# Performance work log

Measured on AMD Instinct MI355X. Metric: run time of the kernel, lower is better.

The kernel has to match this reference:

```python
import jax, jax.numpy as jnp
import numpy as np
from jax import lax

B, N, C, H = 32, 1025, 512, 8
HD = C // H            # head dim = 64
HS = WS = 32           # feature map size, N = 1 + HS*WS
SCALE = HD ** -0.5
SPLITS = (128, 192, 192)  # window {3:2,5:3,7:3} * head_dim


def setup_inputs() -> dict:
    key = jax.random.key(0)
    ks = jax.random.split(key, 11)
    return {
        "x": jax.random.normal(ks[0], (B, N, C), jnp.float32),
        "Wqkv": jax.random.normal(ks[1], (C, 3 * C), jnp.float32) * 0.02,
        "bqkv": jnp.zeros((3 * C,), jnp.float32),
        "Wproj": jax.random.normal(ks[2], (C, C), jnp.float32) * 0.02,
        "bproj": jnp.zeros((C,), jnp.float32),
        "ck3": jax.random.normal(ks[3], (3, 3, 1, SPLITS[0]), jnp.float32) * 0.1,
        "cb3": jnp.zeros((SPLITS[0],), jnp.float32),
        "ck5": jax.random.normal(ks[4], (5, 5, 1, SPLITS[1]), jnp.float32) * 0.1,
        "cb5": jnp.zeros((SPLITS[1],), jnp.float32),
        "ck7": jax.random.normal(ks[5], (7, 7, 1, SPLITS[2]), jnp.float32) * 0.1,
        "cb7": jnp.zeros((SPLITS[2],), jnp.float32),
    }


def _dwconv(x, kern, bias):
    # depthwise conv, Keras Conv2D(groups=C, filters=C, padding='same')
    out = lax.conv_general_dilated(
        x, kern, window_strides=(1, 1), padding="SAME",
        dimension_numbers=("NHWC", "HWIO", "NHWC"),
        feature_group_count=x.shape[-1])
    return out + bias


def reference(x, Wqkv, bqkv, Wproj, bproj, ck3, cb3, ck5, cb5, ck7, cb7):
    # qkv projection: [B,N,3C] -> [B,N,3,H,HD]
    qkv = (x @ Wqkv + bqkv).reshape(B, N, 3, H, HD)
    q, k, v = qkv[:, :, 0], qkv[:, :, 1], qkv[:, :, 2]

    # factorized linear attention: softmax over token axis N
    k_softmax = jax.nn.softmax(k, axis=1)
    ksv = jnp.einsum("bnhk,bnhv->bhkv", k_softmax, v)      # [B,H,HD,HD]
    factor_att = jnp.einsum("bnhk,bhkv->bnhv", q, ksv)     # [B,N,H,HD]

    # conv relative position encoding on image tokens
    v_img = v[:, 1:].reshape(B, HS, WS, C)
    v2, v3, v4 = jnp.split(v_img, np.cumsum(SPLITS)[:-1].tolist(), axis=3)
    conv_v = jnp.concatenate(
        [_dwconv(v2, ck3, cb3), _dwconv(v3, ck5, cb5), _dwconv(v4, ck7, cb7)],
        axis=3).reshape(B, HS * WS, H, HD)
    ev_img = q[:, 1:] * conv_v
    crpe = jnp.concatenate(
        [jnp.zeros((B, 1, H, HD), x.dtype), ev_img], axis=1)  # [B,N,H,HD]

    out = (SCALE * factor_att + crpe).reshape(B, N, C)
    return out @ Wproj + bproj
```

## Files before the change

kernel.cpp:

```cpp
#include <hip/hip_runtime.h>
#include <hip/hip_bf16.h>

#define BB 32
#define NN 1025
#define CC 512
#define HH 8
#define HD 64
#define MM (BB * NN)
#define MP 33024
#define KK 512
#define SCALE 0.125f

typedef unsigned short u16;
typedef __attribute__((ext_vector_type(4))) unsigned short u16x4;
typedef __attribute__((ext_vector_type(8))) unsigned short u16x8;
typedef __attribute__((ext_vector_type(4))) float f32x4;
typedef __attribute__((ext_vector_type(8))) __bf16 bf16x8;

__device__ __forceinline__ u16 f2bf(float f) {
    unsigned u = __float_as_uint(f);
    unsigned r = (u + 0x7FFFu + ((u >> 16) & 1u)) >> 16;
    return (u16)r;
}
__device__ __forceinline__ float bf2f(u16 h) {
    return __uint_as_float((unsigned)h << 16);
}

__device__ __forceinline__ void gload16(const u16* g, u16* l) {
    __builtin_amdgcn_global_load_lds(
        (const __attribute__((address_space(1))) unsigned int*)g,
        (__attribute__((address_space(3))) unsigned int*)l, 16, 0, 0);
}

__global__ __launch_bounds__(256) void convert_x_kernel(
    const float* __restrict__ x, u16* __restrict__ xbf)
{
    size_t t = (size_t)blockIdx.x * 256 + threadIdx.x;
    size_t base = t * 8;
    u16x8 o;
    if (base < (size_t)MM * CC) {
        f32x4 a = *(const f32x4*)&x[base];
        f32x4 b = *(const f32x4*)&x[base + 4];
#pragma unroll
        for (int j = 0; j < 4; j++) { o[j] = f2bf(a[j]); o[j + 4] = f2bf(b[j]); }
    } else {
#pragma unroll
        for (int j = 0; j < 8; j++) o[j] = 0;
    }
    *(u16x8*)&xbf[base] = o;
}

__global__ __launch_bounds__(256) void prep_all_kernel(
    const float* __restrict__ Wqkv, const float* __restrict__ Wproj,
    const float* __restrict__ ck3, const float* __restrict__ cb3,
    const float* __restrict__ ck5, const float* __restrict__ cb5,
    const float* __restrict__ ck7, const float* __restrict__ cb7,
    u16* __restrict__ wqT, u16* __restrict__ wpT,
    float* __restrict__ w7, float* __restrict__ cbx)
{
    int blk = blockIdx.x;
    int tid = threadIdx.x;
    if (blk < 512) {
        const float* W = (blk < 384) ? Wqkv : Wproj;
        u16* Wt = (blk < 384) ? wqT : wpT;
        int N = (blk < 384) ? 1536 : 512;
        int t = (blk < 384 ? blk : blk - 384) * 256 + tid;
        int n = t >> 6;
        int k0 = (t & 63) * 8;
        u16x8 o;
#pragma unroll
        for (int j = 0; j < 8; j++) o[j] = f2bf(W[(size_t)(k0 + j) * N + n]);
        *(u16x8*)&Wt[(size_t)n * KK + k0] = o;
    } else {
        int t = (blk - 512) * 256 + tid;
        if (t >= 49 * 512) return;
        int c = t & 511;
        int tap = t >> 9;
        int dy = tap / 7, dx = tap % 7;
        float w = 0.f;
        if (c < 128) {
            int ry = dy - 2, rx = dx - 2;
            if (ry >= 0 && ry < 3 && rx >= 0 && rx < 3) w = ck3[(ry * 3 + rx) * 128 + c];
        } else if (c < 320) {
            int ry = dy - 1, rx = dx - 1;
            if (ry >= 0 && ry < 5 && rx >= 0 && rx < 5) w = ck5[(ry * 5 + rx) * 192 + (c - 128)];
        } else {
            w = ck7[(dy * 7 + dx) * 192 + (c - 320)];
        }
        w7[tap * 512 + c] = w;
        if (t < 512)
            cbx[t] = (t < 128) ? cb3[t] : (t < 320) ? cb5[t - 128] : cb7[t - 320];
    }
}

template <int MODE, int NSZ, int GX>
__global__ __launch_bounds__(256) void gemm_bf16_kernel(
    const u16* __restrict__ A, const u16* __restrict__ Bt,
    const float* __restrict__ bias, void* __restrict__ outv, int nwg)
{
    __shared__ __align__(16) u16 lds[2][2][4096];

    int wg = blockIdx.x;
    {
        int q = nwg >> 3, r = nwg & 7;
        int xcd = wg & 7, pos = wg >> 3;
        wg = (xcd < r ? xcd * (q + 1) : r * (q + 1) + (xcd - r) * q) + pos;
    }
    const int m0 = (wg / GX) * 128;
    const int n0 = (wg % GX) * 128;

    const int t = threadIdx.x;

    const int srow = t >> 2;
    const int ps   = t & 3;
    const int ls   = ps ^ ((srow >> 1) & 3);
    const u16* gA = A  + (size_t)(m0 + srow) * KK + ls * 8;
    const u16* gB = Bt + (size_t)(n0 + srow) * KK + ls * 8;

    const int l  = t & 63;
    const int w  = t >> 6;
    const int wm = (w >> 1) * 64;
    const int wn = (w & 1) * 64;
    const int lr = l & 15;
    const int s  = l >> 4;
    const int ra = wm + lr;
    const int rb = wn + lr;
    const int offA = ra * 32 + (s ^ ((ra >> 1) & 3)) * 8;
    const int offB = rb * 32 + (s ^ ((rb >> 1) & 3)) * 8;

    f32x4 acc[4][4] = {};

#define STAGE(buf, kk_) do {                                        \
        gload16(gA + (kk_),           &lds[buf][0][t * 8]);         \
        gload16(gA + 64 * KK + (kk_), &lds[buf][0][2048 + t * 8]);  \
        gload16(gB + (kk_),           &lds[buf][1][t * 8]);         \
        gload16(gB + 64 * KK + (kk_), &lds[buf][1][2048 + t * 8]);  \
    } while (0)

    STAGE(0, 0);
    __syncthreads();

    int cur = 0;
    for (int step = 0; step < 16; ++step) {
        if (step < 15) STAGE(cur ^ 1, (step + 1) * 32);
        bf16x8 a[4], b[4];
#pragma unroll
        for (int i = 0; i < 4; i++) a[i] = *(const bf16x8*)&lds[cur][0][offA + i * 512];
#pragma unroll
        for (int i = 0; i < 4; i++) b[i] = *(const bf16x8*)&lds[cur][1][offB + i * 512];
#pragma unroll
        for (int i = 0; i < 4; i++)
#pragma unroll
            for (int j = 0; j < 4; j++)
                acc[i][j] = __builtin_amdgcn_mfma_f32_16x16x32_bf16(a[i], b[j], acc[i][j], 0, 0, 0);
        __syncthreads();
        cur ^= 1;
    }
#undef STAGE

    const int col0 = n0 + wn + lr;
    float bs[4];
#pragma unroll
    for (int j = 0; j < 4; j++) bs[j] = bias[col0 + j * 16];

    if (MODE == 0) {
        u16* eb = &lds[0][0][0];
        const int rl0 = wm + (l >> 4) * 4;
        const int cl0 = wn + lr;
#pragma unroll
        for (int i = 0; i < 4; i++) {
#pragma unroll
            for (int j = 0; j < 4; j++) {
#pragma unroll
                for (int r = 0; r < 4; r++) {
                    int row = rl0 + i * 16 + r;
                    int a_ = (row * 256 + (cl0 + j * 16) * 2) ^ ((row & 12) << 3);
                    eb[a_ >> 1] = f2bf(acc[i][j][r] + bs[j]);
                }
            }
        }
        __syncthreads();
        const int plane = n0 >> 9;
        u16* pl = (u16*)outv + (size_t)plane * ((size_t)MP * CC) + (n0 & 511);
#pragma unroll
        for (int s2 = 0; s2 < 8; s2++) {
            int flat = s2 * 2048 + t * 8;
            int row = flat >> 7, col = flat & 127;
            int a_ = (row * 256 + col * 2) ^ ((row & 12) << 3);
            u16x8 v = *(const u16x8*)((const char*)eb + a_);
            *(u16x8*)&pl[(size_t)(m0 + row) * CC + col] = v;
        }
    } else {
        float* out = (float*)outv;
        const int row0 = m0 + wm + (l >> 4) * 4;
#pragma unroll
        for (int i = 0; i < 4; i++) {
#pragma unroll
            for (int j = 0; j < 4; j++) {
                int gn = col0 + j * 16;
#pragma unroll
                for (int r = 0; r < 4; r++) {
                    int gm = row0 + i * 16 + r;
                    if (gm < MM) out[(size_t)gm * NSZ + gn] = acc[i][j][r] + bs[j];
                }
            }
        }
    }
}

__global__ __launch_bounds__(256) void ksv_part_kernel(
    const u16* __restrict__ kbf, const u16* __restrict__ vbf,
    float* __restrict__ part, float* __restrict__ psum)
{
    int bh = blockIdx.x;
    int chunk = blockIdx.y;
    int b = bh >> 3, h = bh & 7;
    int n0 = chunk * 256;
    int n1 = (chunk == 3) ? NN : n0 + 256;

    __shared__ float ke[16][64];
    __shared__ float ve[16][64];

    int t = threadIdx.x;
    int lrow = t >> 4;
    int lcol = (t & 15) * 4;
    int tx = t & 15, ty = t >> 4;

    float acc[4][4] = {};
    float cs[4] = {};
    for (int nb = n0; nb < n1; nb += 16) {
        int n = nb + lrow;
        bool valid = n < n1;
        size_t off = ((size_t)(b * NN + n)) * CC + h * HD + lcol;
        u16x4 kr = *(const u16x4*)&kbf[off];
        u16x4 vr = *(const u16x4*)&vbf[off];
#pragma unroll
        for (int j = 0; j < 4; j++) {
            ke[lrow][lcol + j] = valid ? __expf(bf2f(kr[j])) : 0.f;
            ve[lrow][lcol + j] = valid ? bf2f(vr[j]) : 0.f;
        }
        __syncthreads();
#pragma unroll 4
        for (int d = 0; d < 16; d++) {
            f32x4 ka = *(const f32x4*)&ke[d][ty * 4];
            f32x4 vb = *(const f32x4*)&ve[d][tx * 4];
#pragma unroll
            for (int i = 0; i < 4; i++)
#pragma unroll
                for (int j = 0; j < 4; j++)
                    acc[i][j] = fmaf(ka[i], vb[j], acc[i][j]);
        }
        if (t < 16) {
#pragma unroll
            for (int d = 0; d < 16; d++) {
                f32x4 kv = *(const f32x4*)&ke[d][t * 4];
#pragma unroll
                for (int j = 0; j < 4; j++) cs[j] += kv[j];
            }
        }
        __syncthreads();
    }

    float* dst = part + ((size_t)chunk * 256 + bh) * 4096;
#pragma unroll
    for (int i = 0; i < 4; i++) {
        f32x4 o = {acc[i][0], acc[i][1], acc[i][2], acc[i][3]};
        *(f32x4*)&dst[(ty * 4 + i) * 64 + tx * 4] = o;
    }
    if (t < 16) {
        f32x4 o = {cs[0], cs[1], cs[2], cs[3]};
        *(f32x4*)&psum[((size_t)chunk * 256 + bh) * 64 + t * 4] = o;
    }
}

__global__ __launch_bounds__(256) void ksv_reduceT_kernel(
    const float* __restrict__ part, const float* __restrict__ psum,
    u16* __restrict__ ksvT)
{
    int i = blockIdx.x * 256 + threadIdx.x;
    size_t e = (size_t)i * 4;
    int bh = (int)(e >> 12);
    int kk = ((int)e >> 6) & 63;
    int vv0 = (int)e & 63;
    f32x4 s = *(const f32x4*)&part[e];
    float cs = psum[bh * 64 + kk];
#pragma unroll
    for (int c = 1; c < 4; c++) {
        f32x4 p = *(const f32x4*)&part[(size_t)c * 256 * 4096 + e];
#pragma unroll
        for (int j = 0; j < 4; j++) s[j] += p[j];
        cs += psum[(size_t)c * 256 * 64 + bh * 64 + kk];
    }
    float inv = SCALE / cs;
#pragma unroll
    for (int j = 0; j < 4; j++)
        ksvT[(size_t)bh * 4096 + (vv0 + j) * 64 + kk] = f2bf(s[j] * inv);
}

__global__ __launch_bounds__(256) void attn_ev_kernel(
    const u16* __restrict__ qbf, const u16* __restrict__ vbf,
    const u16* __restrict__ ksvT, const float* __restrict__ w7,
    const float* __restrict__ cbx, u16* __restrict__ attbf)
{
    int yg = blockIdx.x;
    int bh = blockIdx.y;
    int b = bh >> 3, h = bh & 7;
    int t = threadIdx.x;

    if (yg == 8) {
        if (t < 64) {
            const u16* q0 = qbf + (size_t)(b * NN) * CC + h * HD;
            const u16* kb = ksvT + (size_t)bh * 4096 + t * 64;
            float s = 0.f;
#pragma unroll 8
            for (int kk = 0; kk < 64; kk++)
                s = fmaf(bf2f(q0[kk]), bf2f(kb[kk]), s);
            attbf[(size_t)(b * NN) * CC + h * HD + t] = f2bf(s);
        }
        return;
    }

    const int nbase = 1 + yg * 128;

    __shared__ __align__(16) u16 lq[128 * 64];
    __shared__ __align__(16) u16 lk[64 * 64];
    __shared__ __align__(16) u16 lv[10 * 32 * 64];
    __shared__ __align__(16) u16 latt[128 * 64];

#pragma unroll
    for (int i = 0; i < 4; i++) {
        int idx = t + i * 256;
        int row = idx >> 3, sl = idx & 7;
        u16x8 v = *(const u16x8*)&qbf[((size_t)(b * NN + nbase + row)) * CC + h * HD + sl * 8];
        *(u16x8*)&lq[row * 64 + ((sl ^ (row & 7)) * 8)] = v;
    }
#pragma unroll
    for (int i = 0; i < 2; i++) {
        int idx = t + i * 256;
        int col = idx >> 3, sl = idx & 7;
        u16x8 v = *(const u16x8*)&ksvT[(size_t)bh * 4096 + col * 64 + sl * 8];
        *(u16x8*)&lk[col * 64 + ((col & 7) ^ sl) * 8] = v;
    }
    {
        int x = t >> 3, sl = t & 7;
#pragma unroll
        for (int s = 0; s < 10; s++) {
            int yy = yg * 4 - 3 + s;
            u16x8 v;
            if (yy >= 0 && yy < 32)
                v = *(const u16x8*)&vbf[((size_t)(b * NN) + 1 + yy * 32 + x) * CC + h * HD + sl * 8];
            else {
#pragma unroll
                for (int j = 0; j < 8; j++) v[j] = 0;
            }
            *(u16x8*)&lv[s * 2048 + x * 64 + sl * 8] = v;
        }
    }
    __syncthreads();

    {
        int l = t & 63, w = t >> 6;
        int lr = l & 15, ls = l >> 4;
        f32x4 acc[2][4] = {};
#pragma unroll
        for (int kf = 0; kf < 2; kf++) {
            bf16x8 a[2], bf[4];
#pragma unroll
            for (int i = 0; i < 2; i++) {
                int row = w * 32 + i * 16 + lr;
                a[i] = *(const bf16x8*)&lq[row * 64 + (((kf * 4 + ls) ^ (row & 7)) * 8)];
            }
#pragma unroll
            for (int j = 0; j < 4; j++) {
                int col = j * 16 + lr;
                bf[j] = *(const bf16x8*)&lk[col * 64 + (((kf * 4 + ls) ^ (col & 7)) * 8)];
            }
#pragma unroll
            for (int i = 0; i < 2; i++)
#pragma unroll
                for (int j = 0; j < 4; j++)
                    acc[i][j] = __builtin_amdgcn_mfma_f32_16x16x32_bf16(a[i], bf[j], acc[i][j], 0, 0, 0);
        }
#pragma unroll
        for (int i = 0; i < 2; i++)
#pragma unroll
            for (int j = 0; j < 4; j++)
#pragma unroll
                for (int r = 0; r < 4; r++)
                    latt[(w * 32 + i * 16 + ls * 4 + r) * 64 + j * 16 + lr] =
                        f2bf(acc[i][j][r]);
    }
    __syncthreads();

    int oct = t >> 4;
    int cq = t & 15;
    int c4 = cq * 4;
    int c = h * HD + c4;
    int yo = oct >> 2;
    int x0 = (oct & 3) * 8;

    float a2[8][4];
    {
        f32x4 b0 = *(const f32x4*)&cbx[c];
#pragma unroll
        for (int xi = 0; xi < 8; xi++)
#pragma unroll
            for (int j = 0; j < 4; j++) a2[xi][j] = b0[j];
    }

    for (int dy = 0; dy < 7; dy++) {
        int s = yo + dy;
        float wr[7][4];
#pragma unroll
        for (int dx = 0; dx < 7; dx++)
            *(f32x4*)&wr[dx][0] = *(const f32x4*)&w7[(dy * 7 + dx) * 512 + c];
        u16x4 vv[14];
#pragma unroll
        for (int sxi = 0; sxi < 14; sxi++) {
            int sx = x0 - 3 + sxi;
            int sxc = sx < 0 ? 0 : (sx > 31 ? 31 : sx);
            vv[sxi] = *(const u16x4*)&lv[s * 2048 + sxc * 64 + c4];
        }
#pragma unroll
        for (int sxi = 0; sxi < 14; sxi++) {
            int sx = x0 - 3 + sxi;
            bool xval = (sx >= 0) && (sx < 32);
            float vf[4];
#pragma unroll
            for (int j = 0; j < 4; j++) vf[j] = xval ? bf2f(vv[sxi][j]) : 0.f;
            int lo = sxi - 6 > 0 ? sxi - 6 : 0;
            int hi = sxi < 7 ? sxi : 7;
#pragma unroll
            for (int xi = 0; xi < 8; xi++) {
                if (xi < lo || xi > hi) continue;
                int dx = sxi - xi;
#pragma unroll
                for (int j = 0; j < 4; j++)
                    a2[xi][j] = fmaf(vf[j], wr[dx][j], a2[xi][j]);
            }
        }
    }

#pragma unroll
    for (int xi = 0; xi < 8; xi++) {
        int row = oct * 8 + xi;
        u16x4 at = *(const u16x4*)&latt[row * 64 + c4];
        u16x4 qv = *(const u16x4*)&lq[row * 64 + (((cq >> 1) ^ (row & 7)) * 8) + (cq & 1) * 4];
        u16x4 ov;
#pragma unroll
        for (int j = 0; j < 4; j++)
            ov[j] = f2bf(bf2f(at[j]) + bf2f(qv[j]) * a2[xi][j]);
        *(u16x4*)&attbf[((size_t)(b * NN + nbase + row)) * CC + c] = ov;
    }
}

extern "C" void kernel_launch(void* const* d_in, const int* in_sizes, int n_in,
                              void* d_out, int out_size, void* d_ws, size_t ws_size,
                              hipStream_t stream)
{
    const float* x     = (const float*)d_in[0];
    const float* Wqkv  = (const float*)d_in[1];
    const float* bqkv  = (const float*)d_in[2];
    const float* Wproj = (const float*)d_in[3];
    const float* bproj = (const float*)d_in[4];
    const float* ck3   = (const float*)d_in[5];
    const float* cb3   = (const float*)d_in[6];
    const float* ck5   = (const float*)d_in[7];
    const float* cb5   = (const float*)d_in[8];
    const float* ck7   = (const float*)d_in[9];
    const float* cb7   = (const float*)d_in[10];
    float* out = (float*)d_out;

    const size_t PLANE = (size_t)MP * CC;

    u16* xbf  = (u16*)d_ws;
    u16* qbf  = xbf + PLANE;
    u16* kbf  = qbf + PLANE;
    u16* vbf  = kbf + PLANE;
    u16* wqT  = vbf + PLANE;
    u16* wpT  = wqT + (size_t)1536 * 512;
    u16* ksvT = wpT + (size_t)512 * 512;
    float* psum = (float*)(ksvT + (size_t)256 * 4096);
    float* part = psum + (size_t)4 * 256 * 64;
    float* w7   = part + (size_t)4 * 256 * 4096;
    float* cbx  = w7 + 49 * 512;
    u16* attbf = xbf;

    prep_all_kernel<<<610, 256, 0, stream>>>(
        Wqkv, Wproj, ck3, cb3, ck5, cb5, ck7, cb7, wqT, wpT, w7, cbx);
    convert_x_kernel<<<(int)(PLANE / 8 / 256), 256, 0, stream>>>(x, xbf);

    {
        int nwg = 12 * (MP / 128);
        gemm_bf16_kernel<0, 1536, 12><<<nwg, 256, 0, stream>>>(xbf, wqT, bqkv, qbf, nwg);
    }
    {
        dim3 grid(BB * HH, 4);
        ksv_part_kernel<<<grid, 256, 0, stream>>>(kbf, vbf, part, psum);
        ksv_reduceT_kernel<<<256 * 4096 / 4 / 256, 256, 0, stream>>>(part, psum, ksvT);
    }
    {
        dim3 grid(9, BB * HH);
        attn_ev_kernel<<<grid, 256, 0, stream>>>(qbf, vbf, ksvT, w7, cbx, attbf);
    }
    {
        int nwg = 4 * (MP / 128);
        gemm_bf16_kernel<1, 512, 4><<<nwg, 256, 0, stream>>>(attbf, wpT, bproj, out, nwg);
    }
}
```

Baseline: 231.4 us.

## Fuse prep launches, halve ksv split count, skip zero conv taps per head

Merges the x-to-bf16 conversion and the weight prep into one launch, which removes a kernel launch. Splits the k-softmax·v reduction into 2 chunks instead of 4, so fewer partial buffers are written and read back. In the fused attention/conv kernel, each head now loads and convolves only the rows and columns its real kernel size needs (3, 5 or 7) instead of always a 7x7 window, skipping taps that are zero after padding. The cost is less parallelism in the ksv kernel and divergent loop bounds in the conv.

```diff
diff --git a/kernel.cpp b/kernel.cpp
--- a/kernel.cpp
+++ b/kernel.cpp
@@ -10,6 +10,7 @@
 #define MP 33024
 #define KK 512
 #define SCALE 0.125f
+#define NXB 8256
 
 typedef unsigned short u16;
 typedef __attribute__((ext_vector_type(4))) unsigned short u16x4;
@@ -32,34 +33,34 @@
         (__attribute__((address_space(3))) unsigned int*)l, 16, 0, 0);
 }
 
-__global__ __launch_bounds__(256) void convert_x_kernel(
-    const float* __restrict__ x, u16* __restrict__ xbf)
-{
-    size_t t = (size_t)blockIdx.x * 256 + threadIdx.x;
-    size_t base = t * 8;
-    u16x8 o;
-    if (base < (size_t)MM * CC) {
-        f32x4 a = *(const f32x4*)&x[base];
-        f32x4 b = *(const f32x4*)&x[base + 4];
-#pragma unroll
-        for (int j = 0; j < 4; j++) { o[j] = f2bf(a[j]); o[j + 4] = f2bf(b[j]); }
-    } else {
-#pragma unroll
-        for (int j = 0; j < 8; j++) o[j] = 0;
-    }
-    *(u16x8*)&xbf[base] = o;
-}
-
-__global__ __launch_bounds__(256) void prep_all_kernel(
+__global__ __launch_bounds__(256) void prep_fused_kernel(
+    const float* __restrict__ x,
     const float* __restrict__ Wqkv, const float* __restrict__ Wproj,
     const float* __restrict__ ck3, const float* __restrict__ cb3,
     const float* __restrict__ ck5, const float* __restrict__ cb5,
     const float* __restrict__ ck7, const float* __restrict__ cb7,
-    u16* __restrict__ wqT, u16* __restrict__ wpT,
+    u16* __restrict__ xbf, u16* __restrict__ wqT, u16* __restrict__ wpT,
     float* __restrict__ w7, float* __restrict__ cbx)
 {
     int blk = blockIdx.x;
     int tid = threadIdx.x;
+    if (blk < NXB) {
+        size_t t = (size_t)blk * 256 + tid;
+        size_t base = t * 8;
+        u16x8 o;
+        if (base < (size_t)MM * CC) {
+            f32x4 a = *(const f32x4*)&x[base];
+            f32x4 b = *(const f32x4*)&x[base + 4];
+#pragma unroll
+            for (int j = 0; j < 4; j++) { o[j] = f2bf(a[j]); o[j + 4] = f2bf(b[j]); }
+        } else {
+#pragma unroll
+            for (int j = 0; j < 8; j++) o[j] = 0;
+        }
+        *(u16x8*)&xbf[base] = o;
+        return;
+    }
+    blk -= NXB;
     if (blk < 512) {
         const float* W = (blk < 384) ? Wqkv : Wproj;
         u16* Wt = (blk < 384) ? wqT : wpT;
@@ -215,8 +216,8 @@
     int bh = blockIdx.x;
     int chunk = blockIdx.y;
     int b = bh >> 3, h = bh & 7;
-    int n0 = chunk * 256;
-    int n1 = (chunk == 3) ? NN : n0 + 256;
+    int n0 = chunk * 512;
+    int n1 = chunk ? NN : 512;
 
     __shared__ float ke[16][64];
     __shared__ float ve[16][64];
@@ -284,12 +285,11 @@
     int vv0 = (int)e & 63;
     f32x4 s = *(const f32x4*)&part[e];
     float cs = psum[bh * 64 + kk];
-#pragma unroll
-    for (int c = 1; c < 4; c++) {
-        f32x4 p = *(const f32x4*)&part[(size_t)c * 256 * 4096 + e];
+    {
+        f32x4 p = *(const f32x4*)&part[(size_t)256 * 4096 + e];
 #pragma unroll
         for (int j = 0; j < 4; j++) s[j] += p[j];
-        cs += psum[(size_t)c * 256 * 64 + bh * 64 + kk];
+        cs += psum[(size_t)256 * 64 + bh * 64 + kk];
     }
     float inv = SCALE / cs;
 #pragma unroll
@@ -320,6 +320,7 @@
         return;
     }
 
+    const int pad = (h < 2) ? 1 : (h < 5) ? 2 : 3;
     const int nbase = 1 + yg * 128;
 
     __shared__ __align__(16) u16 lq[128 * 64];
@@ -343,8 +344,10 @@
     }
     {
         int x = t >> 3, sl = t & 7;
+        int slo = 3 - pad, shi = 6 + pad;
 #pragma unroll
         for (int s = 0; s < 10; s++) {
+            if (s < slo || s > shi) continue;
             int yy = yg * 4 - 3 + s;
             u16x8 v;
             if (yy >= 0 && yy < 32)
@@ -408,26 +411,23 @@
             for (int j = 0; j < 4; j++) a2[xi][j] = b0[j];
     }
 
-    for (int dy = 0; dy < 7; dy++) {
+    const int sxlo = 3 - pad, sxhi = 10 + pad;
+    for (int dy = 3 - pad; dy <= 3 + pad; dy++) {
         int s = yo + dy;
         float wr[7][4];
 #pragma unroll
         for (int dx = 0; dx < 7; dx++)
             *(f32x4*)&wr[dx][0] = *(const f32x4*)&w7[(dy * 7 + dx) * 512 + c];
-        u16x4 vv[14];
 #pragma unroll
         for (int sxi = 0; sxi < 14; sxi++) {
+            if (sxi < sxlo || sxi > sxhi) continue;
             int sx = x0 - 3 + sxi;
             int sxc = sx < 0 ? 0 : (sx > 31 ? 31 : sx);
-            vv[sxi] = *(const u16x4*)&lv[s * 2048 + sxc * 64 + c4];
-        }
-#pragma unroll
-        for (int sxi = 0; sxi < 14; sxi++) {
-            int sx = x0 - 3 + sxi;
+            u16x4 vv = *(const u16x4*)&lv[s * 2048 + sxc * 64 + c4];
             bool xval = (sx >= 0) && (sx < 32);
             float vf[4];
 #pragma unroll
-            for (int j = 0; j < 4; j++) vf[j] = xval ? bf2f(vv[sxi][j]) : 0.f;
+            for (int j = 0; j < 4; j++) vf[j] = xval ? bf2f(vv[j]) : 0.f;
             int lo = sxi - 6 > 0 ? sxi - 6 : 0;
             int hi = sxi < 7 ? sxi : 7;
 #pragma unroll
@@ -481,21 +481,20 @@
     u16* wpT  = wqT + (size_t)1536 * 512;
     u16* ksvT = wpT + (size_t)512 * 512;
     float* psum = (float*)(ksvT + (size_t)256 * 4096);
-    float* part = psum + (size_t)4 * 256 * 64;
-    float* w7   = part + (size_t)4 * 256 * 4096;
+    float* part = psum + (size_t)2 * 256 * 64;
+    float* w7   = part + (size_t)2 * 256 * 4096;
     float* cbx  = w7 + 49 * 512;
     u16* attbf = xbf;
 
-    prep_all_kernel<<<610, 256, 0, stream>>>(
-        Wqkv, Wproj, ck3, cb3, ck5, cb5, ck7, cb7, wqT, wpT, w7, cbx);
-    convert_x_kernel<<<(int)(PLANE / 8 / 256), 256, 0, stream>>>(x, xbf);
+    prep_fused_kernel<<<NXB + 610, 256, 0, stream>>>(
+        x, Wqkv, Wproj, ck3, cb3, ck5, cb5, ck7, cb7, xbf, wqT, wpT, w7, cbx);
 
     {
         int nwg = 12 * (MP / 128);
         gemm_bf16_kernel<0, 1536, 12><<<nwg, 256, 0, stream>>>(xbf, wqT, bqkv, qbf, nwg);
     }
     {
-        dim3 grid(BB * HH, 4);
+        dim3 grid(BB * HH, 2);
         ksv_part_kernel<<<grid, 256, 0, stream>>>(kbf, vbf, part, psum);
         ksv_reduceT_kernel<<<256 * 4096 / 4 / 256, 256, 0, stream>>>(part, psum, ksvT);
     }
```

After: 237.4 us. 2.6% more time.
